# Kernel optimization log

Hardware: AMD Instinct MI355X
Metric: run time of the kernel (lower is better)

Reference implementation:

```python
import jax, jax.numpy as jnp
import numpy as np

# SDNet-CTRL cfg constants
MU = 0.1          # FISTA step size (cfg['MODEL']['MU'])
LMBD = 0.1        # sparsity weight (cfg['MODEL']['LAMBDA'][0])
N_STEPS = 4       # FISTA iterations (cfg['MODEL']['NUM_LAYERS'])
EPS_BN = 1e-5


def _conv(x, w, stride, padding):
    # torch F.conv2d, NCHW / OIHW
    return jax.lax.conv_general_dilated(
        x, w, window_strides=(stride, stride),
        padding=[(padding, padding), (padding, padding)],
        dimension_numbers=('NCHW', 'OIHW', 'NCHW'))


def _conv_t(c, w, stride, padding):
    # torch F.conv_transpose2d(c, w, stride, padding) with output_padding chosen
    # so that it exactly inverts the spatial map of _conv (k=4,s=2,p=1 -> 0).
    k = w.shape[2]
    w_t = jnp.flip(w, (2, 3)).transpose(1, 0, 2, 3)  # (I,O,k,k) flipped
    pad = k - 1 - padding
    return jax.lax.conv_general_dilated(
        c, w_t, window_strides=(1, 1),
        padding=[(pad, pad), (pad, pad)],
        lhs_dilation=(stride, stride),
        dimension_numbers=('NCHW', 'OIHW', 'NCHW'))


def _shrink_nn(c, thr):
    # non-negative soft threshold (cfg NONEGATIVE=True)
    return jax.nn.relu(c - thr)


def _dict_conv(x, w, stride, padding):
    # DictBlock: FISTA convolutional sparse coding, n_dict=1, w_norm=True.
    # normalize each dictionary atom (output filter) to unit l2 norm
    wn = w * jax.lax.rsqrt(jnp.sum(w * w, axis=(1, 2, 3), keepdims=True))
    ss = MU
    thr = LMBD * ss
    # t = 0
    c = _shrink_nn(ss * _conv(x, wn, stride, padding), thr)
    c_pre_pre = jnp.zeros_like(c)
    c_pre = c
    tk = 1.0
    for t in range(1, N_STEPS):
        tk_pre = tk
        tk = (1.0 + float(np.sqrt(1.0 + 4.0 * tk_pre * tk_pre))) / 2.0
        y = c_pre + ((tk_pre - 1.0) / tk) * (c_pre - c_pre_pre)
        r = x - _conv_t(y, wn, stride, padding)      # residual in image space
        c = _shrink_nn(y + ss * _conv(r, wn, stride, padding), thr)
        c_pre_pre, c_pre = c_pre, c
    return c


def _bn(x, g, b):
    # training-mode BatchNorm2d (batch statistics)
    m = jnp.mean(x, axis=(0, 2, 3), keepdims=True)
    v = jnp.var(x, axis=(0, 2, 3), keepdims=True)
    return g.reshape(1, -1, 1, 1) * (x - m) * jax.lax.rsqrt(v + EPS_BN) + b.reshape(1, -1, 1, 1)


def _lrelu(x):
    return jnp.where(x >= 0, x, 0.2 * x)


def setup_inputs() -> dict:
    key = jax.random.key(0)
    ks = jax.random.split(key, 5)
    nc, ndf, nz = 3, 128, 256
    B, H = 256, 32

    def mk_w(k, o, i):
        return jax.random.normal(k, (o, i, 4, 4), jnp.float32) * 0.02

    return {
        'x': jax.random.normal(ks[0], (B, nc, H, H), jnp.float32),
        'w1': mk_w(ks[1], ndf, nc),
        'w2': mk_w(ks[2], 2 * ndf, ndf),
        'w3': mk_w(ks[3], 4 * ndf, 2 * ndf),
        'w4': mk_w(ks[4], nz, 4 * ndf),
        'g2': jnp.ones((2 * ndf,), jnp.float32),
        'b2': jnp.zeros((2 * ndf,), jnp.float32),
        'g3': jnp.ones((4 * ndf,), jnp.float32),
        'b3': jnp.zeros((4 * ndf,), jnp.float32),
    }


def reference(x, w1, w2, w3, w4, g2, b2, g3, b3):
    h = _lrelu(_dict_conv(x, w1, 2, 1))                 # (B, ndf, 16, 16)
    h = _lrelu(_bn(_dict_conv(h, w2, 2, 1), g2, b2))    # (B, 2ndf, 8, 8)
    h = _lrelu(_bn(_dict_conv(h, w3, 2, 1), g3, b3))    # (B, 4ndf, 4, 4)
    h = _dict_conv(h, w4, 1, 0)                         # (B, nz, 1, 1)
    h = h.reshape(h.shape[0], -1)                       # Flatten
    n = jnp.sqrt(jnp.sum(h * h, axis=1, keepdims=True))
    return h / jnp.maximum(n, 1e-12)                    # F.normalize(dim=1)
```

## Files before the change

kernel.cpp:

```cpp
#include <hip/hip_runtime.h>
#include <math.h>

#define SS   0.1f
#define THRC 0.01f

typedef __attribute__((ext_vector_type(8))) short s16x8;
typedef __attribute__((ext_vector_type(4))) float f32x4;

__device__ __forceinline__ float b2f(unsigned short u){
  union{unsigned int i; float f;} v; v.i = ((unsigned int)u)<<16; return v.f;
}
__device__ __forceinline__ unsigned short f2b(float f){
  union{float f; unsigned int i;} v; v.f = f;
  return (unsigned short)((v.i + 0x7fffu + ((v.i>>16)&1u))>>16);
}
__device__ __forceinline__ s16x8 as_s16x8(uint4 u){
  union{uint4 a; s16x8 b;} c; c.a = u; return c.b;
}
__device__ __forceinline__ int swz8(int row, int q){ return (row<<3) | (q ^ (row&7)); }

enum { EPI_FIRST=0, EPI_UPDATE=1, EPI_PARTIAL=2, EPI_RES_NHWC=3, EPI_RES_FLAT=4 };

struct EpiM {
  unsigned short* C;
  const unsigned short* Y;
  const unsigned short* Cprev;
  unsigned short* Yout;
  const unsigned short* img;
  float coef;
  int lH, lW, lC;
  int S_MN, Kc;
};

struct LA_ident {
  const unsigned short* A; int K;
  __device__ void setz(int){}
  __device__ __forceinline__ uint4 ld(int m, int k8) const {
    return *(const uint4*)(A + (size_t)m*K + ((size_t)k8<<3));
  }
};
struct LA_nhwc {
  const unsigned short* img; int lH, lW, lC;
  __device__ void setz(int){}
  __device__ __forceinline__ uint4 ld(int m, int k8) const {
    int lWo = lW-1, lHo = lH-1;
    int wo = m & ((1<<lWo)-1); int t = m>>lWo; int ho = t & ((1<<lHo)-1); int b = t>>lHo;
    int k = k8<<3; int kk = k>>lC; int i = k & ((1<<lC)-1);
    int kw = kk&3, kh = kk>>2;
    int h = 2*ho + kh - 1, w = 2*wo + kw - 1;
    if ((unsigned)h >= (1u<<lH) || (unsigned)w >= (1u<<lW)) return make_uint4(0,0,0,0);
    return *(const uint4*)(img + (((((((size_t)b<<lH)|h)<<lW)|w))<<lC) + i);
  }
};
struct LA_yg {
  const unsigned short* y; int lHo, lWo, lO, ph, pw;
  __device__ void setz(int z){ ph = z>>1; pw = z&1; }
  __device__ __forceinline__ uint4 ld(int m, int k8) const {
    int l = m & ((1<<lWo)-1); int t = m>>lWo; int j = t & ((1<<lHo)-1); int b = t>>lHo;
    int k = k8<<3; int tt = k>>lO; int o = k & ((1<<lO)-1);
    int th = tt>>1, tw = tt&1;
    int ho = ph ? (j+1-th) : (j-th);
    int wo = pw ? (l+1-tw) : (l-tw);
    if ((unsigned)ho >= (1u<<lHo) || (unsigned)wo >= (1u<<lWo)) return make_uint4(0,0,0,0);
    return *(const uint4*)(y + (((((((size_t)b<<lHo)|ho)<<lWo)|wo))<<lO) + o);
  }
};
struct LA_pad {
  const float* img;
  __device__ void setz(int){}
  __device__ __forceinline__ uint4 ld(int m, int k8) const {
    int wo = m&15, t = m>>4, ho = t&15, b = t>>4;
    int kh = k8>>1, kw0 = (k8&1)<<1;
    int h = 2*ho + kh, w = 2*wo + kw0;
    const float* p = img + (((size_t)b*34 + h)*34 + w)*4;
    float4 A0 = *(const float4*)p;
    float4 A1 = *(const float4*)(p+4);
    union{unsigned short s[8]; uint4 u;} r;
    r.s[0]=f2b(A0.x); r.s[1]=f2b(A0.y); r.s[2]=f2b(A0.z); r.s[3]=f2b(A0.w);
    r.s[4]=f2b(A1.x); r.s[5]=f2b(A1.y); r.s[6]=f2b(A1.z); r.s[7]=f2b(A1.w);
    return r.u;
  }
};

template<class AL, int EPI>
__global__ __launch_bounds__(512)
void mgemm_k(AL al, const unsigned short* __restrict__ Bw, int M, int N, int K, EpiM ep)
{
  __shared__ uint4 As[1024];
  __shared__ uint4 Bs[1024];
  const int tid = threadIdx.x;
  const int bm = blockIdx.y<<7, bn = blockIdx.x<<7;
  const int z = blockIdx.z;
  int kb = 0, ke = K;
  const unsigned short* Bp = Bw;
  if (EPI == EPI_PARTIAL){ kb = z*ep.Kc; ke = kb + ep.Kc; }
  if (EPI == EPI_RES_NHWC){ Bp = Bw + (size_t)z*(size_t)N*K; al.setz(z); }

  f32x4 acc[4][2];
  #pragma unroll
  for (int i=0;i<4;++i)
    #pragma unroll
    for (int j=0;j<2;++j){ acc[i][j][0]=0.f; acc[i][j][1]=0.f; acc[i][j][2]=0.f; acc[i][j][3]=0.f; }

  const int lane = tid & 63, wid = tid >> 6;
  const int wm = (wid>>2)<<6, wn = (wid&3)<<5;
  const int fr = lane & 15, fq = lane >> 4;
  const int sr = tid>>3, sq = tid&7;

  for (int k0 = kb; k0 < ke; k0 += 64){
    int k8 = k0>>3;
    As[swz8(sr,   sq)] = al.ld(bm+sr,    k8+sq);
    As[swz8(sr+64,sq)] = al.ld(bm+sr+64, k8+sq);
    {
      int gn0 = bn+sr, gn1 = bn+sr+64;
      uint4 b0 = make_uint4(0,0,0,0), b1 = make_uint4(0,0,0,0);
      if (gn0 < N) b0 = *(const uint4*)(Bp + (size_t)gn0*K + k0 + (sq<<3));
      if (gn1 < N) b1 = *(const uint4*)(Bp + (size_t)gn1*K + k0 + (sq<<3));
      Bs[swz8(sr,   sq)] = b0;
      Bs[swz8(sr+64,sq)] = b1;
    }
    __syncthreads();
    #pragma unroll
    for (int half=0; half<2; ++half){
      const int qb = (half<<2) | fq;
      s16x8 af[4], bf[2];
      #pragma unroll
      for (int mi=0;mi<4;++mi) af[mi] = as_s16x8(As[swz8(wm + mi*16 + fr, qb)]);
      #pragma unroll
      for (int ni=0;ni<2;++ni) bf[ni] = as_s16x8(Bs[swz8(wn + ni*16 + fr, qb)]);
      #pragma unroll
      for (int mi=0;mi<4;++mi)
        #pragma unroll
        for (int ni=0;ni<2;++ni)
          acc[mi][ni] = __builtin_amdgcn_mfma_f32_16x16x32_bf16(af[mi], bf[ni], acc[mi][ni], 0,0,0);
    }
    __syncthreads();
  }

  #pragma unroll
  for (int mi=0;mi<4;++mi){
    #pragma unroll
    for (int ni=0;ni<2;++ni){
      int n = bn + wn + ni*16 + fr;
      if (n >= N) continue;
      int mb = bm + wm + mi*16 + (fq<<2);
      #pragma unroll
      for (int r=0;r<4;++r){
        int m = mb + r;
        float a = acc[mi][ni][r];
        if (EPI == EPI_FIRST){
          float v = SS*a - THRC; v = v>0.f ? v : 0.f;
          ep.C[(size_t)m*N + n] = f2b(v);
        } else if (EPI == EPI_UPDATE){
          size_t idx = (size_t)m*N + n;
          float v = b2f(ep.Y[idx]) + SS*a - THRC; v = v>0.f ? v : 0.f;
          ep.C[idx] = f2b(v);
          if (ep.Yout) ep.Yout[idx] = f2b(v + ep.coef*(v - b2f(ep.Cprev[idx])));
        } else if (EPI == EPI_PARTIAL){
          ep.C[(size_t)z*ep.S_MN + (size_t)m*N + n] = f2b(a);
        } else if (EPI == EPI_RES_NHWC){
          int lWo = ep.lW-1, lHo = ep.lH-1;
          int l = m & ((1<<lWo)-1); int t = m>>lWo; int j = t & ((1<<lHo)-1); int b = t>>lHo;
          int h = 2*j + (z>>1), w = 2*l + (z&1);
          size_t ridx = (((((((size_t)b<<ep.lH)|h)<<ep.lW)|w))<<ep.lC) | n;
          ep.C[ridx] = f2b(b2f(ep.img[ridx]) - a);
        } else {
          size_t ridx = (size_t)m*N + n;
          ep.C[ridx] = f2b(b2f(ep.img[ridx]) - a);
        }
      }
    }
  }
}

__global__ __launch_bounds__(64)
void wnorm1_k(const float* __restrict__ w, unsigned short* __restrict__ wf1,
              unsigned short* __restrict__ wcolT)
{
  int o = blockIdx.x, tid = threadIdx.x;
  __shared__ float red[64];
  float v = (tid < 48) ? w[(size_t)o*48 + tid] : 0.f;
  red[tid] = v*v; __syncthreads();
  for (int d=32; d>0; d>>=1){ if (tid<d) red[tid] += red[tid+d]; __syncthreads(); }
  float nv = v * rsqrtf(red[0]);
  if (tid < 48){
    int c = tid>>4, t = tid&15;
    wf1[(size_t)o*64 + t*4 + c] = f2b(nv);
    wcolT[(size_t)(t*4+c)*128 + o] = f2b(nv);
  } else {
    int t = tid - 48;
    wf1[(size_t)o*64 + t*4 + 3] = 0;
    wcolT[(size_t)(t*4+3)*128 + o] = 0;
  }
}
__global__ __launch_bounds__(256)
void wnormX_k(const float* __restrict__ w, int Cin, int O,
              unsigned short* __restrict__ wT, unsigned short* __restrict__ wclsT,
              unsigned short* __restrict__ wEO)
{
  int o = blockIdx.x, tid = threadIdx.x; int E = Cin*16;
  __shared__ float red[256];
  float s = 0.f;
  for (int e = tid; e < E; e += 256){ float v = w[(size_t)o*E + e]; s += v*v; }
  red[tid] = s; __syncthreads();
  for (int d=128; d>0; d>>=1){ if (tid<d) red[tid] += red[tid+d]; __syncthreads(); }
  float scale = rsqrtf(red[0]);
  for (int e = tid; e < E; e += 256){
    float v = w[(size_t)o*E + e] * scale;
    int i = e>>4, t = e&15, kh = t>>2, kw = t&3;
    int ee = t*Cin + i;
    if (wT)  wT[(size_t)o*E + ee] = f2b(v);
    if (wEO) wEO[(size_t)ee*O + o] = f2b(v);
    if (wclsT){
      int ph = (kh&1)^1, pw = (kw&1)^1, cls = ph*2+pw;
      int tt = (kh>>1)*2 + (kw>>1);
      wclsT[(((size_t)cls*Cin + i)*4 + tt)*O + o] = f2b(v);
    }
  }
}

__global__ void splitk_shrink_k(const unsigned short* __restrict__ part,
                                const unsigned short* __restrict__ Y,
                                unsigned short* __restrict__ C,
                                unsigned short* __restrict__ Yout,
                                const unsigned short* __restrict__ Cprev,
                                float coef, int MN, int S)
{
  for (int i = blockIdx.x*blockDim.x + threadIdx.x; i < MN; i += gridDim.x*blockDim.x){
    float s = 0.f;
    for (int zz = 0; zz < S; ++zz) s += b2f(part[(size_t)zz*MN + i]);
    float v = (Y ? b2f(Y[i]) : 0.f) + SS*s - THRC; v = v>0.f ? v : 0.f;
    C[i] = f2b(v);
    if (Yout) Yout[i] = f2b(v + coef*(v - b2f(Cprev[i])));
  }
}

__global__ void pad_x_k(const float* __restrict__ x, float* __restrict__ xp){
  int idx = blockIdx.x*256 + threadIdx.x;
  if (idx >= 262144) return;
  int w = idx&31, t = idx>>5, h = t&31, b = t>>5;
  size_t src = (size_t)b*3072 + h*32 + w;
  float* d = xp + (((size_t)b*34 + h+1)*34 + w+1)*4;
  d[0] = x[src]; d[1] = x[src+1024]; d[2] = x[src+2048];
}

__global__ void l1_resid_k(const unsigned short* __restrict__ Col,
                           const float* __restrict__ x, float* __restrict__ r1p)
{
  int idx = blockIdx.x*256 + threadIdx.x;
  if (idx >= 262144) return;
  int w = idx&31, t = idx>>5, h = t&31, b = t>>5;
  float a0=0.f, a1=0.f, a2=0.f;
  #pragma unroll
  for (int kh=0; kh<4; ++kh){
    int hh = h+1-kh; if (hh & 1) continue; int ho = hh>>1; if ((unsigned)ho >= 16u) continue;
    #pragma unroll
    for (int kw=0; kw<4; ++kw){
      int ww = w+1-kw; if (ww & 1) continue; int wo = ww>>1; if ((unsigned)wo >= 16u) continue;
      int m = (b*16+ho)*16+wo;
      const unsigned short* cp = Col + (size_t)m*64 + (kh*4+kw)*4;
      a0 += b2f(cp[0]); a1 += b2f(cp[1]); a2 += b2f(cp[2]);
    }
  }
  size_t src = (size_t)b*3072 + h*32 + w;
  float* d = r1p + (((size_t)b*34 + h+1)*34 + w+1)*4;
  d[0] = x[src] - a0; d[1] = x[src+1024] - a1; d[2] = x[src+2048] - a2;
}

__global__ void bn_stats_k(const unsigned short* __restrict__ d, float* __restrict__ sums,
                           int rows, int O){
  for (int c = threadIdx.x; c < O; c += blockDim.x){
    float a = 0.f, b = 0.f;
    for (int r = blockIdx.x; r < rows; r += gridDim.x){
      float v = b2f(d[(size_t)r*O + c]); a += v; b += v*v;
    }
    atomicAdd(&sums[c], a); atomicAdd(&sums[O+c], b);
  }
}
__global__ void bn_apply_k(const unsigned short* __restrict__ d, const float* __restrict__ sums,
                           const float* __restrict__ g, const float* __restrict__ bta,
                           unsigned short* __restrict__ outp, int rows, int O, float inv_cnt){
  int total = rows*O;
  for (int i = blockIdx.x*blockDim.x + threadIdx.x; i < total; i += gridDim.x*blockDim.x){
    int c = i % O;
    float mean = sums[c]*inv_cnt;
    float var  = sums[O+c]*inv_cnt - mean*mean;
    float v = g[c]*(b2f(d[i])-mean)*rsqrtf(var + 1e-5f) + bta[c];
    outp[i] = f2b(v >= 0.f ? v : 0.2f*v);
  }
}

__global__ __launch_bounds__(256)
void norm_rows_k(const unsigned short* __restrict__ h, float* __restrict__ out){
  int row = blockIdx.x, tid = threadIdx.x;
  __shared__ float red[256];
  float v = b2f(h[(size_t)row*256 + tid]);
  red[tid] = v*v; __syncthreads();
  for (int d=128; d>0; d>>=1){ if (tid<d) red[tid] += red[tid+d]; __syncthreads(); }
  float nrm = sqrtf(red[0]); nrm = nrm > 1e-12f ? nrm : 1e-12f;
  out[(size_t)row*256 + tid] = v / nrm;
}

extern "C" void kernel_launch(void* const* d_in, const int* in_sizes, int n_in,
                              void* d_out, int out_size, void* d_ws, size_t ws_size,
                              hipStream_t stream)
{
  const float* x  = (const float*)d_in[0];
  const float* w1 = (const float*)d_in[1];
  const float* w2 = (const float*)d_in[2];
  const float* w3 = (const float*)d_in[3];
  const float* w4 = (const float*)d_in[4];
  const float* g2 = (const float*)d_in[5];
  const float* b2 = (const float*)d_in[6];
  const float* g3 = (const float*)d_in[7];
  const float* b3 = (const float*)d_in[8];
  float* out = (float*)d_out;

  char* p = (char*)d_ws;
  auto ah = [&](size_t n){ unsigned short* r = (unsigned short*)p; p += n*2; return r; };
  auto af = [&](size_t n){ float* r = (float*)p; p += n*4; return r; };

  unsigned short* wf1    = ah(128*64);
  unsigned short* wcol1T = ah(64*128);
  unsigned short* wT2    = ah((size_t)256*2048);
  unsigned short* wcls2  = ah((size_t)4*128*1024);
  unsigned short* wT3    = ah((size_t)512*4096);
  unsigned short* wcls3  = ah((size_t)4*256*2048);
  unsigned short* wT4    = ah((size_t)256*8192);
  unsigned short* wE4    = ah((size_t)8192*256);
  unsigned short* h1     = ah((size_t)8388608);
  unsigned short* h2     = ah((size_t)4194304);
  unsigned short* h3     = ah((size_t)2097152);
  unsigned short* cA     = ah((size_t)8388608);
  unsigned short* cB     = ah((size_t)8388608);
  unsigned short* yA     = ah((size_t)8388608);
  unsigned short* yB     = ah((size_t)8388608);
  unsigned short* rH     = ah((size_t)8388608);
  char* regionA = p; p += 17858560;
  unsigned short* Col    = (unsigned short*)regionA;
  float*          xp     = (float*)(regionA + 8388608);
  float*          r1p    = (float*)(regionA + 8388608 + 4734976);
  unsigned short* partL3 = (unsigned short*)regionA;
  unsigned short* partL4 = (unsigned short*)regionA;
  float* bnsum = af(1024);

  double tk = 1.0; float coef[4] = {0.f,0.f,0.f,0.f};
  for (int t = 1; t < 4; ++t){
    double tkp = tk; tk = (1.0 + sqrt(1.0 + 4.0*tkp*tkp))*0.5;
    coef[t] = (float)((tkp - 1.0)/tk);
  }

  hipMemsetAsync(xp,  0, 4734976, stream);
  hipMemsetAsync(r1p, 0, 4734976, stream);
  pad_x_k<<<1024,256,0,stream>>>(x, xp);
  wnorm1_k<<<128, 64, 0, stream>>>(w1, wf1, wcol1T);
  wnormX_k<<<256,256,0,stream>>>(w2, 128, 256, wT2, wcls2, nullptr);
  wnormX_k<<<512,256,0,stream>>>(w3, 256, 512, wT3, wcls3, nullptr);
  wnormX_k<<<256,256,0,stream>>>(w4, 512, 256, wT4, nullptr, wE4);

  auto l1_fwd = [&](const float* src, const unsigned short* Y, const unsigned short* Cp,
                    unsigned short* Cout, unsigned short* Yout, float cf){
    LA_pad al{src};
    EpiM ep{}; ep.C=Cout; ep.Y=Y; ep.Cprev=Cp; ep.Yout=Yout; ep.coef=cf;
    dim3 g(1, 512, 1);
    if (Y) mgemm_k<LA_pad,EPI_UPDATE><<<g,512,0,stream>>>(al, wf1, 65536,128,64, ep);
    else   mgemm_k<LA_pad,EPI_FIRST ><<<g,512,0,stream>>>(al, wf1, 65536,128,64, ep);
  };
  auto l1_tconv = [&](const unsigned short* y){
    LA_ident al{y, 128};
    EpiM ep{}; ep.C=Col; ep.S_MN=0; ep.Kc=128;
    mgemm_k<LA_ident,EPI_PARTIAL><<<dim3(1,512,1),512,0,stream>>>(al, wcol1T, 65536,64,128, ep);
    l1_resid_k<<<1024,256,0,stream>>>(Col, x, r1p);
  };
  l1_fwd(xp,  nullptr, nullptr, cA, nullptr, 0.f);
  l1_tconv(cA);
  l1_fwd(r1p, cA, cA, cB, yA, coef[2]);
  l1_tconv(yA);
  l1_fwd(r1p, yA, cB, cA, yB, coef[3]);
  l1_tconv(yB);
  l1_fwd(r1p, yB, nullptr, h1, nullptr, 0.f);

  auto l2_fwd = [&](const unsigned short* src, const unsigned short* Y, const unsigned short* Cp,
                    unsigned short* Cout, unsigned short* Yout, float cf){
    LA_nhwc al{src, 4,4,7};
    EpiM ep{}; ep.C=Cout; ep.Y=Y; ep.Cprev=Cp; ep.Yout=Yout; ep.coef=cf;
    dim3 g(2, 128, 1);
    if (Y) mgemm_k<LA_nhwc,EPI_UPDATE><<<g,512,0,stream>>>(al, wT2, 16384,256,2048, ep);
    else   mgemm_k<LA_nhwc,EPI_FIRST ><<<g,512,0,stream>>>(al, wT2, 16384,256,2048, ep);
  };
  auto l2_tconv = [&](const unsigned short* y){
    LA_yg al{y, 3,3,8, 0,0};
    EpiM ep{}; ep.C=rH; ep.img=h1; ep.lH=4; ep.lW=4; ep.lC=7;
    mgemm_k<LA_yg,EPI_RES_NHWC><<<dim3(1,128,4),512,0,stream>>>(al, wcls2, 16384,128,1024, ep);
  };
  l2_fwd(h1, nullptr, nullptr, cA, nullptr, 0.f);
  l2_tconv(cA);
  l2_fwd(rH, cA, cA, cB, yA, coef[2]);
  l2_tconv(yA);
  l2_fwd(rH, yA, cB, cA, yB, coef[3]);
  l2_tconv(yB);
  l2_fwd(rH, yB, nullptr, cB, nullptr, 0.f);
  hipMemsetAsync(bnsum, 0, 2*256*sizeof(float), stream);
  bn_stats_k<<<256,256,0,stream>>>(cB, bnsum, 16384, 256);
  bn_apply_k<<<2048,256,0,stream>>>(cB, bnsum, g2, b2, h2, 16384, 256, 1.f/16384.f);

  auto l3_fwd = [&](const unsigned short* src, const unsigned short* Y, const unsigned short* Cp,
                    unsigned short* Cout, unsigned short* Yout, float cf){
    LA_nhwc al{src, 3,3,8};
    EpiM ep{}; ep.C=partL3; ep.S_MN=4096*512; ep.Kc=1024;
    mgemm_k<LA_nhwc,EPI_PARTIAL><<<dim3(4,32,4),512,0,stream>>>(al, wT3, 4096,512,4096, ep);
    splitk_shrink_k<<<1024,256,0,stream>>>(partL3, Y, Cout, Yout, Cp, cf, 4096*512, 4);
  };
  auto l3_tconv = [&](const unsigned short* y){
    LA_yg al{y, 2,2,9, 0,0};
    EpiM ep{}; ep.C=rH; ep.img=h2; ep.lH=3; ep.lW=3; ep.lC=8;
    mgemm_k<LA_yg,EPI_RES_NHWC><<<dim3(2,32,4),512,0,stream>>>(al, wcls3, 4096,256,2048, ep);
  };
  l3_fwd(h2, nullptr, nullptr, cA, nullptr, 0.f);
  l3_tconv(cA);
  l3_fwd(rH, cA, cA, cB, yA, coef[2]);
  l3_tconv(yA);
  l3_fwd(rH, yA, cB, cA, yB, coef[3]);
  l3_tconv(yB);
  l3_fwd(rH, yB, nullptr, cB, nullptr, 0.f);
  hipMemsetAsync(bnsum, 0, 2*512*sizeof(float), stream);
  bn_stats_k<<<256,256,0,stream>>>(cB, bnsum, 4096, 512);
  bn_apply_k<<<2048,256,0,stream>>>(cB, bnsum, g3, b3, h3, 4096, 512, 1.f/4096.f);

  auto l4_fwd = [&](const unsigned short* Asrc, const unsigned short* Y, const unsigned short* Cp,
                    unsigned short* Cout, unsigned short* Yout, float cf){
    LA_ident al{Asrc, 8192};
    EpiM ep{}; ep.C=partL4; ep.S_MN=65536; ep.Kc=256;
    mgemm_k<LA_ident,EPI_PARTIAL><<<dim3(2,2,32),512,0,stream>>>(al, wT4, 256,256,8192, ep);
    splitk_shrink_k<<<256,256,0,stream>>>(partL4, Y, Cout, Yout, Cp, cf, 65536, 32);
  };
  auto l4_tconv = [&](const unsigned short* y){
    LA_ident al{y, 256};
    EpiM ep{}; ep.C=rH; ep.img=h3;
    mgemm_k<LA_ident,EPI_RES_FLAT><<<dim3(64,2,1),512,0,stream>>>(al, wE4, 256,8192,256, ep);
  };
  l4_fwd(h3, nullptr, nullptr, cA, nullptr, 0.f);
  l4_tconv(cA);
  l4_fwd(rH, cA, cA, cB, yA, coef[2]);
  l4_tconv(yA);
  l4_fwd(rH, yA, cB, cA, yB, coef[3]);
  l4_tconv(yB);
  l4_fwd(rH, yB, nullptr, cB, nullptr, 0.f);

  norm_rows_k<<<256,256,0,stream>>>(cB, out);
}
```

Measured before the change: 1.020 ms.

## Double-buffer shared memory tiles and prefetch next K-slice into registers

The MFMA GEMM main loop now keeps two LDS buffers for the A and B tiles. It issues the global loads for the next K step into registers before computing on the current buffer, so one barrier per iteration replaces two and global latency overlaps with MFMA work. In exchange the kernel uses twice the shared memory (64 KB per block) and more registers, which may lower occupancy. Correctness relies on the single barrier plus buffer alternation preventing write-after-read hazards.

```diff
diff --git a/kernel.cpp b/kernel.cpp
--- a/kernel.cpp
+++ b/kernel.cpp
@@ -86,8 +86,8 @@
 __global__ __launch_bounds__(512)
 void mgemm_k(AL al, const unsigned short* __restrict__ Bw, int M, int N, int K, EpiM ep)
 {
-  __shared__ uint4 As[1024];
-  __shared__ uint4 Bs[1024];
+  __shared__ uint4 As[2048];
+  __shared__ uint4 Bs[2048];
   const int tid = threadIdx.x;
   const int bm = blockIdx.y<<7, bn = blockIdx.x<<7;
   const int z = blockIdx.z;
@@ -106,35 +106,46 @@
   const int wm = (wid>>2)<<6, wn = (wid&3)<<5;
   const int fr = lane & 15, fq = lane >> 4;
   const int sr = tid>>3, sq = tid&7;
-
+  const int gn0 = bn+sr, gn1 = bn+sr+64;
+
+  uint4 ra0, ra1, rb0, rb1;
+  auto fetch = [&](int k0){
+    int k8 = k0>>3;
+    ra0 = al.ld(bm+sr,    k8+sq);
+    ra1 = al.ld(bm+sr+64, k8+sq);
+    uint4 b0 = make_uint4(0,0,0,0), b1 = make_uint4(0,0,0,0);
+    if (gn0 < N) b0 = *(const uint4*)(Bp + (size_t)gn0*K + k0 + (sq<<3));
+    if (gn1 < N) b1 = *(const uint4*)(Bp + (size_t)gn1*K + k0 + (sq<<3));
+    rb0 = b0; rb1 = b1;
+  };
+
+  fetch(kb);
+  int buf = 0;
   for (int k0 = kb; k0 < ke; k0 += 64){
-    int k8 = k0>>3;
-    As[swz8(sr,   sq)] = al.ld(bm+sr,    k8+sq);
-    As[swz8(sr+64,sq)] = al.ld(bm+sr+64, k8+sq);
-    {
-      int gn0 = bn+sr, gn1 = bn+sr+64;
-      uint4 b0 = make_uint4(0,0,0,0), b1 = make_uint4(0,0,0,0);
-      if (gn0 < N) b0 = *(const uint4*)(Bp + (size_t)gn0*K + k0 + (sq<<3));
-      if (gn1 < N) b1 = *(const uint4*)(Bp + (size_t)gn1*K + k0 + (sq<<3));
-      Bs[swz8(sr,   sq)] = b0;
-      Bs[swz8(sr+64,sq)] = b1;
-    }
-    __syncthreads();
+    const int base = buf<<10;
+    As[base | swz8(sr,   sq)] = ra0;
+    As[base | swz8(sr+64,sq)] = ra1;
+    Bs[base | swz8(sr,   sq)] = rb0;
+    Bs[base | swz8(sr+64,sq)] = rb1;
+    if (k0 + 64 < ke) fetch(k0 + 64);
+    asm volatile("s_waitcnt lgkmcnt(0)" ::: "memory");
+    __builtin_amdgcn_s_barrier();
+    __builtin_amdgcn_sched_barrier(0);
     #pragma unroll
     for (int half=0; half<2; ++half){
       const int qb = (half<<2) | fq;
       s16x8 af[4], bf[2];
       #pragma unroll
-      for (int mi=0;mi<4;++mi) af[mi] = as_s16x8(As[swz8(wm + mi*16 + fr, qb)]);
+      for (int mi=0;mi<4;++mi) af[mi] = as_s16x8(As[base | swz8(wm + mi*16 + fr, qb)]);
       #pragma unroll
-      for (int ni=0;ni<2;++ni) bf[ni] = as_s16x8(Bs[swz8(wn + ni*16 + fr, qb)]);
+      for (int ni=0;ni<2;++ni) bf[ni] = as_s16x8(Bs[base | swz8(wn + ni*16 + fr, qb)]);
       #pragma unroll
       for (int mi=0;mi<4;++mi)
         #pragma unroll
         for (int ni=0;ni<2;++ni)
           acc[mi][ni] = __builtin_amdgcn_mfma_f32_16x16x32_bf16(af[mi], bf[ni], acc[mi][ni], 0,0,0);
     }
-    __syncthreads();
+    buf ^= 1;
   }
 
   #pragma unroll
```

Result: faster. 888.5 us (-12.9%).

## Double-buffer GEMM tiles with direct global-to-LDS loads and bf16 layer-1 input

Applied to the files above, without the earlier changes.

The shared GEMM kernel now fetches A and B tiles with global_load_lds straight into a double-buffered LDS array, issuing the next k-tile before computing the current one. This replaces register-staged stores and two barriers per step with one wait plus one barrier. Out-of-bounds rows now point at a zeroed scratch buffer instead of returning zeros. The padded layer-1 input and residual are stored as bf16 rather than fp32, which removes per-load conversion and halves that traffic. The cost is double the LDS per block (64 KB), which can lower occupancy, and the barrier placement needs the single vmcnt wait to be correct.

```diff
diff --git a/kernel.cpp b/kernel.cpp
--- a/kernel.cpp
+++ b/kernel.cpp
@@ -18,6 +18,12 @@
   union{uint4 a; s16x8 b;} c; c.a = u; return c.b;
 }
 __device__ __forceinline__ int swz8(int row, int q){ return (row<<3) | (q ^ (row&7)); }
+
+__device__ __forceinline__ void gld16(const void* g, void* l){
+  __builtin_amdgcn_global_load_lds(
+      (const __attribute__((address_space(1))) unsigned int*)g,
+      (__attribute__((address_space(3))) unsigned int*)l, 16, 0, 0);
+}
 
 enum { EPI_FIRST=0, EPI_UPDATE=1, EPI_PARTIAL=2, EPI_RES_NHWC=3, EPI_RES_FLAT=4 };
 
@@ -27,6 +33,7 @@
   const unsigned short* Cprev;
   unsigned short* Yout;
   const unsigned short* img;
+  const unsigned short* zp;
   float coef;
   int lH, lW, lC;
   int S_MN, Kc;
@@ -35,50 +42,44 @@
 struct LA_ident {
   const unsigned short* A; int K;
   __device__ void setz(int){}
-  __device__ __forceinline__ uint4 ld(int m, int k8) const {
-    return *(const uint4*)(A + (size_t)m*K + ((size_t)k8<<3));
+  __device__ __forceinline__ const unsigned short* addr(int m, int k8) const {
+    return A + (size_t)m*K + ((size_t)k8<<3);
   }
 };
 struct LA_nhwc {
-  const unsigned short* img; int lH, lW, lC;
+  const unsigned short* img; const unsigned short* zp; int lH, lW, lC;
   __device__ void setz(int){}
-  __device__ __forceinline__ uint4 ld(int m, int k8) const {
+  __device__ __forceinline__ const unsigned short* addr(int m, int k8) const {
     int lWo = lW-1, lHo = lH-1;
     int wo = m & ((1<<lWo)-1); int t = m>>lWo; int ho = t & ((1<<lHo)-1); int b = t>>lHo;
     int k = k8<<3; int kk = k>>lC; int i = k & ((1<<lC)-1);
     int kw = kk&3, kh = kk>>2;
     int h = 2*ho + kh - 1, w = 2*wo + kw - 1;
-    if ((unsigned)h >= (1u<<lH) || (unsigned)w >= (1u<<lW)) return make_uint4(0,0,0,0);
-    return *(const uint4*)(img + (((((((size_t)b<<lH)|h)<<lW)|w))<<lC) + i);
+    if ((unsigned)h >= (1u<<lH) || (unsigned)w >= (1u<<lW)) return zp;
+    return img + (((((((size_t)b<<lH)|h)<<lW)|w))<<lC) + i;
   }
 };
 struct LA_yg {
-  const unsigned short* y; int lHo, lWo, lO, ph, pw;
+  const unsigned short* y; const unsigned short* zp; int lHo, lWo, lO, ph, pw;
   __device__ void setz(int z){ ph = z>>1; pw = z&1; }
-  __device__ __forceinline__ uint4 ld(int m, int k8) const {
+  __device__ __forceinline__ const unsigned short* addr(int m, int k8) const {
     int l = m & ((1<<lWo)-1); int t = m>>lWo; int j = t & ((1<<lHo)-1); int b = t>>lHo;
     int k = k8<<3; int tt = k>>lO; int o = k & ((1<<lO)-1);
     int th = tt>>1, tw = tt&1;
     int ho = ph ? (j+1-th) : (j-th);
     int wo = pw ? (l+1-tw) : (l-tw);
-    if ((unsigned)ho >= (1u<<lHo) || (unsigned)wo >= (1u<<lWo)) return make_uint4(0,0,0,0);
-    return *(const uint4*)(y + (((((((size_t)b<<lHo)|ho)<<lWo)|wo))<<lO) + o);
+    if ((unsigned)ho >= (1u<<lHo) || (unsigned)wo >= (1u<<lWo)) return zp;
+    return y + (((((((size_t)b<<lHo)|ho)<<lWo)|wo))<<lO) + o;
   }
 };
-struct LA_pad {
-  const float* img;
+struct LA_padb {
+  const unsigned short* img;
   __device__ void setz(int){}
-  __device__ __forceinline__ uint4 ld(int m, int k8) const {
+  __device__ __forceinline__ const unsigned short* addr(int m, int k8) const {
     int wo = m&15, t = m>>4, ho = t&15, b = t>>4;
     int kh = k8>>1, kw0 = (k8&1)<<1;
     int h = 2*ho + kh, w = 2*wo + kw0;
-    const float* p = img + (((size_t)b*34 + h)*34 + w)*4;
-    float4 A0 = *(const float4*)p;
-    float4 A1 = *(const float4*)(p+4);
-    union{unsigned short s[8]; uint4 u;} r;
-    r.s[0]=f2b(A0.x); r.s[1]=f2b(A0.y); r.s[2]=f2b(A0.z); r.s[3]=f2b(A0.w);
-    r.s[4]=f2b(A1.x); r.s[5]=f2b(A1.y); r.s[6]=f2b(A1.z); r.s[7]=f2b(A1.w);
-    return r.u;
+    return img + (((size_t)b*34 + h)*34 + w)*4;
   }
 };
 
@@ -86,8 +87,7 @@
 __global__ __launch_bounds__(512)
 void mgemm_k(AL al, const unsigned short* __restrict__ Bw, int M, int N, int K, EpiM ep)
 {
-  __shared__ uint4 As[1024];
-  __shared__ uint4 Bs[1024];
+  __shared__ uint4 S[2][2048];
   const int tid = threadIdx.x;
   const int bm = blockIdx.y<<7, bn = blockIdx.x<<7;
   const int z = blockIdx.z;
@@ -105,21 +105,34 @@
   const int lane = tid & 63, wid = tid >> 6;
   const int wm = (wid>>2)<<6, wn = (wid&3)<<5;
   const int fr = lane & 15, fq = lane >> 4;
-  const int sr = tid>>3, sq = tid&7;
-
+
+  auto issue = [&](int k0, int b){
+    int k8 = k0>>3;
+    #pragma unroll
+    for (int i=0;i<2;++i){
+      int s  = (wid<<7) + (i<<6) + lane;
+      int sr = s>>3, q = (s&7) ^ (sr&7);
+      gld16(al.addr(bm+sr, k8+q), (void*)&S[b][(wid<<7) + (i<<6)]);
+    }
+    #pragma unroll
+    for (int i=0;i<2;++i){
+      int s  = (wid<<7) + (i<<6) + lane;
+      int sr = s>>3, q = (s&7) ^ (sr&7);
+      int gn = bn + sr;
+      const unsigned short* src = (gn < N) ? Bp + (size_t)gn*K + ((size_t)(k8+q)<<3) : ep.zp;
+      gld16(src, (void*)&S[b][1024 + (wid<<7) + (i<<6)]);
+    }
+  };
+
+  issue(kb, 0);
+  int buf = 0;
   for (int k0 = kb; k0 < ke; k0 += 64){
-    int k8 = k0>>3;
-    As[swz8(sr,   sq)] = al.ld(bm+sr,    k8+sq);
-    As[swz8(sr+64,sq)] = al.ld(bm+sr+64, k8+sq);
-    {
-      int gn0 = bn+sr, gn1 = bn+sr+64;
-      uint4 b0 = make_uint4(0,0,0,0), b1 = make_uint4(0,0,0,0);
-      if (gn0 < N) b0 = *(const uint4*)(Bp + (size_t)gn0*K + k0 + (sq<<3));
-      if (gn1 < N) b1 = *(const uint4*)(Bp + (size_t)gn1*K + k0 + (sq<<3));
-      Bs[swz8(sr,   sq)] = b0;
-      Bs[swz8(sr+64,sq)] = b1;
-    }
-    __syncthreads();
+    asm volatile("s_waitcnt vmcnt(0)" ::: "memory");
+    __builtin_amdgcn_s_barrier();
+    __builtin_amdgcn_sched_barrier(0);
+    if (k0 + 64 < ke) issue(k0 + 64, buf^1);
+    const uint4* As = &S[buf][0];
+    const uint4* Bs = &S[buf][1024];
     #pragma unroll
     for (int half=0; half<2; ++half){
       const int qb = (half<<2) | fq;
@@ -134,7 +147,7 @@
         for (int ni=0;ni<2;++ni)
           acc[mi][ni] = __builtin_amdgcn_mfma_f32_16x16x32_bf16(af[mi], bf[ni], acc[mi][ni], 0,0,0);
     }
-    __syncthreads();
+    buf ^= 1;
   }
 
   #pragma unroll
@@ -235,17 +248,17 @@
   }
 }
 
-__global__ void pad_x_k(const float* __restrict__ x, float* __restrict__ xp){
+__global__ void pad_x_k(const float* __restrict__ x, unsigned short* __restrict__ xpb){
   int idx = blockIdx.x*256 + threadIdx.x;
   if (idx >= 262144) return;
   int w = idx&31, t = idx>>5, h = t&31, b = t>>5;
   size_t src = (size_t)b*3072 + h*32 + w;
-  float* d = xp + (((size_t)b*34 + h+1)*34 + w+1)*4;
-  d[0] = x[src]; d[1] = x[src+1024]; d[2] = x[src+2048];
+  unsigned short* d = xpb + (((size_t)b*34 + h+1)*34 + w+1)*4;
+  d[0] = f2b(x[src]); d[1] = f2b(x[src+1024]); d[2] = f2b(x[src+2048]); d[3] = 0;
 }
 
 __global__ void l1_resid_k(const unsigned short* __restrict__ Col,
-                           const float* __restrict__ x, float* __restrict__ r1p)
+                           const float* __restrict__ x, unsigned short* __restrict__ r1pb)
 {
   int idx = blockIdx.x*256 + threadIdx.x;
   if (idx >= 262144) return;
@@ -263,8 +276,8 @@
     }
   }
   size_t src = (size_t)b*3072 + h*32 + w;
-  float* d = r1p + (((size_t)b*34 + h+1)*34 + w+1)*4;
-  d[0] = x[src] - a0; d[1] = x[src+1024] - a1; d[2] = x[src+2048] - a2;
+  unsigned short* d = r1pb + (((size_t)b*34 + h+1)*34 + w+1)*4;
+  d[0] = f2b(x[src] - a0); d[1] = f2b(x[src+1024] - a1); d[2] = f2b(x[src+2048] - a2); d[3] = 0;
 }
 
 __global__ void bn_stats_k(const unsigned short* __restrict__ d, float* __restrict__ sums,
@@ -338,11 +351,12 @@
   unsigned short* rH     = ah((size_t)8388608);
   char* regionA = p; p += 17858560;
   unsigned short* Col    = (unsigned short*)regionA;
-  float*          xp     = (float*)(regionA + 8388608);
-  float*          r1p    = (float*)(regionA + 8388608 + 4734976);
+  unsigned short* xpb    = (unsigned short*)(regionA + 8388608);
+  unsigned short* r1pb   = (unsigned short*)(regionA + 8388608 + 2367488);
   unsigned short* partL3 = (unsigned short*)regionA;
   unsigned short* partL4 = (unsigned short*)regionA;
   float* bnsum = af(1024);
+  unsigned short* zp16 = ah(128);
 
   double tk = 1.0; float coef[4] = {0.f,0.f,0.f,0.f};
   for (int t = 1; t < 4; ++t){
@@ -350,47 +364,48 @@
     coef[t] = (float)((tkp - 1.0)/tk);
   }
 
-  hipMemsetAsync(xp,  0, 4734976, stream);
-  hipMemsetAsync(r1p, 0, 4734976, stream);
-  pad_x_k<<<1024,256,0,stream>>>(x, xp);
+  hipMemsetAsync(zp16, 0, 256, stream);
+  hipMemsetAsync(xpb,  0, 2367488, stream);
+  hipMemsetAsync(r1pb, 0, 2367488, stream);
+  pad_x_k<<<1024,256,0,stream>>>(x, xpb);
   wnorm1_k<<<128, 64, 0, stream>>>(w1, wf1, wcol1T);
   wnormX_k<<<256,256,0,stream>>>(w2, 128, 256, wT2, wcls2, nullptr);
   wnormX_k<<<512,256,0,stream>>>(w3, 256, 512, wT3, wcls3, nullptr);
   wnormX_k<<<256,256,0,stream>>>(w4, 512, 256, wT4, nullptr, wE4);
 
-  auto l1_fwd = [&](const float* src, const unsigned short* Y, const unsigned short* Cp,
+  auto l1_fwd = [&](const unsigned short* src, const unsigned short* Y, const unsigned short* Cp,
                     unsigned short* Cout, unsigned short* Yout, float cf){
-    LA_pad al{src};
-    EpiM ep{}; ep.C=Cout; ep.Y=Y; ep.Cprev=Cp; ep.Yout=Yout; ep.coef=cf;
+    LA_padb al{src};
+    EpiM ep{}; ep.C=Cout; ep.Y=Y; ep.Cprev=Cp; ep.Yout=Yout; ep.coef=cf; ep.zp=zp16;
     dim3 g(1, 512, 1);
-    if (Y) mgemm_k<LA_pad,EPI_UPDATE><<<g,512,0,stream>>>(al, wf1, 65536,128,64, ep);
-    else   mgemm_k<LA_pad,EPI_FIRST ><<<g,512,0,stream>>>(al, wf1, 65536,128,64, ep);
+    if (Y) mgemm_k<LA_padb,EPI_UPDATE><<<g,512,0,stream>>>(al, wf1, 65536,128,64, ep);
+    else   mgemm_k<LA_padb,EPI_FIRST ><<<g,512,0,stream>>>(al, wf1, 65536,128,64, ep);
   };
   auto l1_tconv = [&](const unsigned short* y){
     LA_ident al{y, 128};
-    EpiM ep{}; ep.C=Col; ep.S_MN=0; ep.Kc=128;
+    EpiM ep{}; ep.C=Col; ep.S_MN=0; ep.Kc=128; ep.zp=zp16;
     mgemm_k<LA_ident,EPI_PARTIAL><<<dim3(1,512,1),512,0,stream>>>(al, wcol1T, 65536,64,128, ep);
-    l1_resid_k<<<1024,256,0,stream>>>(Col, x, r1p);
-  };
-  l1_fwd(xp,  nullptr, nullptr, cA, nullptr, 0.f);
+    l1_resid_k<<<1024,256,0,stream>>>(Col, x, r1pb);
+  };
+  l1_fwd(xpb,  nullptr, nullptr, cA, nullptr, 0.f);
   l1_tconv(cA);
-  l1_fwd(r1p, cA, cA, cB, yA, coef[2]);
+  l1_fwd(r1pb, cA, cA, cB, yA, coef[2]);
   l1_tconv(yA);
-  l1_fwd(r1p, yA, cB, cA, yB, coef[3]);
+  l1_fwd(r1pb, yA, cB, cA, yB, coef[3]);
   l1_tconv(yB);
-  l1_fwd(r1p, yB, nullptr, h1, nullptr, 0.f);
+  l1_fwd(r1pb, yB, nullptr, h1, nullptr, 0.f);
 
   auto l2_fwd = [&](const unsigned short* src, const unsigned short* Y, const unsigned short* Cp,
                     unsigned short* Cout, unsigned short* Yout, float cf){
-    LA_nhwc al{src, 4,4,7};
-    EpiM ep{}; ep.C=Cout; ep.Y=Y; ep.Cprev=Cp; ep.Yout=Yout; ep.coef=cf;
+    LA_nhwc al{src, zp16, 4,4,7};
+    EpiM ep{}; ep.C=Cout; ep.Y=Y; ep.Cprev=Cp; ep.Yout=Yout; ep.coef=cf; ep.zp=zp16;
     dim3 g(2, 128, 1);
     if (Y) mgemm_k<LA_nhwc,EPI_UPDATE><<<g,512,0,stream>>>(al, wT2, 16384,256,2048, ep);
     else   mgemm_k<LA_nhwc,EPI_FIRST ><<<g,512,0,stream>>>(al, wT2, 16384,256,2048, ep);
   };
   auto l2_tconv = [&](const unsigned short* y){
-    LA_yg al{y, 3,3,8, 0,0};
-    EpiM ep{}; ep.C=rH; ep.img=h1; ep.lH=4; ep.lW=4; ep.lC=7;
+    LA_yg al{y, zp16, 3,3,8, 0,0};
+    EpiM ep{}; ep.C=rH; ep.img=h1; ep.lH=4; ep.lW=4; ep.lC=7; ep.zp=zp16;
     mgemm_k<LA_yg,EPI_RES_NHWC><<<dim3(1,128,4),512,0,stream>>>(al, wcls2, 16384,128,1024, ep);
   };
   l2_fwd(h1, nullptr, nullptr, cA, nullptr, 0.f);
@@ -406,14 +421,14 @@
 
   auto l3_fwd = [&](const unsigned short* src, const unsigned short* Y, const unsigned short* Cp,
                     unsigned short* Cout, unsigned short* Yout, float cf){
-    LA_nhwc al{src, 3,3,8};
-    EpiM ep{}; ep.C=partL3; ep.S_MN=4096*512; ep.Kc=1024;
+    LA_nhwc al{src, zp16, 3,3,8};
+    EpiM ep{}; ep.C=partL3; ep.S_MN=4096*512; ep.Kc=1024; ep.zp=zp16;
     mgemm_k<LA_nhwc,EPI_PARTIAL><<<dim3(4,32,4),512,0,stream>>>(al, wT3, 4096,512,4096, ep);
     splitk_shrink_k<<<1024,256,0,stream>>>(partL3, Y, Cout, Yout, Cp, cf, 4096*512, 4);
   };
   auto l3_tconv = [&](const unsigned short* y){
-    LA_yg al{y, 2,2,9, 0,0};
-    EpiM ep{}; ep.C=rH; ep.img=h2; ep.lH=3; ep.lW=3; ep.lC=8;
+    LA_yg al{y, zp16, 2,2,9, 0,0};
+    EpiM ep{}; ep.C=rH; ep.img=h2; ep.lH=3; ep.lW=3; ep.lC=8; ep.zp=zp16;
     mgemm_k<LA_yg,EPI_RES_NHWC><<<dim3(2,32,4),512,0,stream>>>(al, wcls3, 4096,256,2048, ep);
   };
   l3_fwd(h2, nullptr, nullptr, cA, nullptr, 0.f);
@@ -430,13 +445,13 @@
   auto l4_fwd = [&](const unsigned short* Asrc, const unsigned short* Y, const unsigned short* Cp,
                     unsigned short* Cout, unsigned short* Yout, float cf){
     LA_ident al{Asrc, 8192};
-    EpiM ep{}; ep.C=partL4; ep.S_MN=65536; ep.Kc=256;
+    EpiM ep{}; ep.C=partL4; ep.S_MN=65536; ep.Kc=256; ep.zp=zp16;
     mgemm_k<LA_ident,EPI_PARTIAL><<<dim3(2,2,32),512,0,stream>>>(al, wT4, 256,256,8192, ep);
     splitk_shrink_k<<<256,256,0,stream>>>(partL4, Y, Cout, Yout, Cp, cf, 65536, 32);
   };
   auto l4_tconv = [&](const unsigned short* y){
     LA_ident al{y, 256};
-    EpiM ep{}; ep.C=rH; ep.img=h3;
+    EpiM ep{}; ep.C=rH; ep.img=h3; ep.zp=zp16;
     mgemm_k<LA_ident,EPI_RES_FLAT><<<dim3(64,2,1),512,0,stream>>>(al, wE4, 256,8192,256, ep);
   };
   l4_fwd(h3, nullptr, nullptr, cA, nullptr, 0.f);
```

Result: faster. 889.3 us (-12.8%).
